# Performance work log

Measured on AMD Instinct MI355X. Metric: run time of the kernel, lower is better.

Reference implementation:

```python
import jax, jax.numpy as jnp
import numpy as np

B, S, E = 4, 2048, 768
DFF = 4 * E
EPS = 1e-5


def _layernorm(x, g, b):
    mu = jnp.mean(x, axis=-1, keepdims=True)
    var = jnp.mean(jnp.square(x - mu), axis=-1, keepdims=True)
    return (x - mu) * jax.lax.rsqrt(var + EPS) * g + b


def setup_inputs() -> dict:
    key = jax.random.key(0)
    ks = jax.random.split(key, 16)
    w = lambda k, shp: jax.random.normal(k, shp, dtype=jnp.float32) * 0.02
    inp = {
        "x": jax.random.normal(ks[0], (B, S, E), dtype=jnp.float32),
        "kv": jax.random.normal(ks[1], (B, S, E), dtype=jnp.float32),
        "wq_w": w(ks[2], (E, E)), "wq_b": jnp.zeros((E,), jnp.float32),
        "wk_w": w(ks[3], (E, E)), "wk_b": jnp.zeros((E,), jnp.float32),
        "wv_w": w(ks[4], (E, E)), "wv_b": jnp.zeros((E,), jnp.float32),
        "ln1_g": jnp.ones((E,), jnp.float32), "ln1_b": jnp.zeros((E,), jnp.float32),
        "wq2_w": w(ks[5], (E, E)), "wq2_b": jnp.zeros((E,), jnp.float32),
        "wk2_w": w(ks[6], (E, E)), "wk2_b": jnp.zeros((E,), jnp.float32),
        "wv2_w": w(ks[7], (E, E)), "wv2_b": jnp.zeros((E,), jnp.float32),
        "ln2_g": jnp.ones((E,), jnp.float32), "ln2_b": jnp.zeros((E,), jnp.float32),
        "w1": w(ks[8], (DFF, E)), "b1": jnp.zeros((DFF,), jnp.float32),
        "w2": w(ks[9], (E, DFF)), "b2": jnp.zeros((E,), jnp.float32),
        "ln3_g": jnp.ones((E,), jnp.float32), "ln3_b": jnp.zeros((E,), jnp.float32),
    }
    return inp


def reference(x, kv, wq_w, wq_b, wk_w, wk_b, wv_w, wv_b, ln1_g, ln1_b,
              wq2_w, wq2_b, wk2_w, wk2_b, wv2_w, wv2_b, ln2_g, ln2_b,
              w1, b1, w2, b2, ln3_g, ln3_b):
    scalar = 1.0 / np.sqrt(E).astype(np.float32)
    mask_value = jnp.finfo(x.dtype).min
    s = x.shape[1]
    causal = jnp.triu(jnp.ones((s, s), dtype=bool), k=1)  # True above diagonal -> masked

    # ---- causal self-attention (single head, full E) ----
    q = x @ wq_w.T + wq_b
    k = x @ wk_w.T + wk_b
    v = x @ wv_w.T + wv_b
    scores = jnp.einsum('bqe,bke->bqk', q, k) * scalar
    scores = jnp.where(causal, mask_value, scores)
    h1 = jnp.einsum('bqk,bke->bqe', jax.nn.softmax(scores, axis=-1), v)
    x = _layernorm(x + h1, ln1_g, ln1_b)

    # ---- cross-attention over kv (no mask) ----
    q2 = x @ wq2_w.T + wq2_b
    k2 = kv @ wk2_w.T + wk2_b
    v2 = kv @ wv2_w.T + wv2_b
    scores2 = jnp.einsum('bqe,bke->bqk', q2, k2) * scalar
    h2 = jnp.einsum('bqk,bke->bqe', jax.nn.softmax(scores2, axis=-1), v2)
    x = _layernorm(x + h2, ln2_g, ln2_b)

    # ---- MLP: Linear -> ReLU -> Linear -> ReLU (note trailing ReLU) ----
    h = jax.nn.relu(x @ w1.T + b1)
    mlp = jax.nn.relu(h @ w2.T + b2)
    return _layernorm(x + mlp, ln3_g, ln3_b)
```

## Files before the change

kernel.cpp:

```cpp
#include <hip/hip_runtime.h>
#include <hip/hip_bf16.h>
#include <math.h>


typedef __bf16 bf16_t;
typedef bf16_t bf16x4 __attribute__((ext_vector_type(4)));
typedef bf16_t bf16x8 __attribute__((ext_vector_type(8)));
typedef float f32x4 __attribute__((ext_vector_type(4)));

struct MMDesc {
    const bf16_t* A;
    const bf16_t* B;
    const float* bias;
    __hip_bfloat16* C;
    float* lsum;
    int koff;
    int trans;
};
struct MMArgs { MMDesc g[8]; };

__device__ __forceinline__ int xcd_swz(int bid, int nwg) {
    const int q = nwg >> 3, r = nwg & 7;
    const int xcd = bid & 7, o = bid >> 3;
    const int base = (xcd < r) ? xcd * (q + 1) : r * (q + 1) + (xcd - r) * q;
    return base + o;
}

__device__ __forceinline__ void load16(const bf16_t* g, bf16_t* l) {
    __builtin_amdgcn_global_load_lds(
        (const __attribute__((address_space(1))) unsigned int*)g,
        (__attribute__((address_space(3))) unsigned int*)l, 16, 0, 0);
}

#define SBAR asm volatile("s_barrier" ::: "memory")
#define SCH  __builtin_amdgcn_sched_barrier(0)
#define PRIO1 __builtin_amdgcn_s_setprio(1)
#define PRIO0 __builtin_amdgcn_s_setprio(0)
#define VMC0 asm volatile("s_waitcnt vmcnt(0)" ::: "memory")

#define RDA(dst, base, H) do { \
    _Pragma("unroll") \
    for (int i_ = 0; i_ < 4; ++i_) \
        dst[i_] = *(const bf16x8*)((base) + (H) + i_ * 1024); \
} while (0)
#define RDB(dst, base) do { \
    dst[0] = *(const bf16x8*)(base); \
    dst[1] = *(const bf16x8*)((base) + 1024); \
    dst[2] = *(const bf16x8*)((base) + 8192); \
    dst[3] = *(const bf16x8*)((base) + 8192 + 1024); \
} while (0)
#define CL16(mh, A_, B_) do { \
    _Pragma("unroll") \
    for (int mi = 0; mi < 4; ++mi) \
    _Pragma("unroll") \
    for (int nj = 0; nj < 4; ++nj) \
        acc[(mh) * 4 + mi][nj] = __builtin_amdgcn_mfma_f32_16x16x32_bf16( \
            A_[mi], B_[nj], acc[(mh) * 4 + mi][nj], 0, 0, 0); \
} while (0)
#define PH(nr) do { \
    __builtin_amdgcn_sched_group_barrier(0x100, nr, 0); \
    __builtin_amdgcn_sched_group_barrier(0x008, 16, 0); \
    SCH; \
} while (0)

__device__ __forceinline__ void mm8_core(
    const bf16_t* Ag, const bf16_t* Bg, int lda, int ldb, int K,
    bf16_t* lds, int w, int l, f32x4 acc[8][4])
{
    const long ldal = lda, ldbl = ldb;
    const int fr = l & 15, kq = l >> 4;
    const int rr = w * 8 + (l >> 3);
    const int c8e = ((l & 7) ^ (l >> 3)) * 8;
    const bf16_t* pA[2];
    const bf16_t* pB[2];
    pA[0] = Ag + (long)rr * ldal + c8e;
    pA[1] = pA[0] + 128 * ldal;
    pB[0] = Bg + (long)rr * ldbl + c8e;
    pB[1] = pB[0] + 128 * ldbl;
    const int s0 = ((0 + kq) ^ (fr & 7)) * 8;
    const int s1 = ((4 + kq) ^ (fr & 7)) * 8;
    const int arow = ((w >> 2) * 64 + fr) * 64;
    const int brow = ((w & 3) * 32 + fr) * 64;
    const bf16_t* A00 = lds + arow + s0;
    const bf16_t* A01 = lds + arow + s1;
    const bf16_t* A10 = lds + 32768 + arow + s0;
    const bf16_t* A11 = lds + 32768 + arow + s1;
    const bf16_t* B00 = lds + 16384 + brow + s0;
    const bf16_t* B01 = lds + 16384 + brow + s1;
    const bf16_t* B10 = lds + 49152 + brow + s0;
    const bf16_t* B11 = lds + 49152 + brow + s1;
    bf16_t* stA = lds + w * 512;
    bf16_t* stB = lds + 16384 + w * 512;

    auto stg = [&](int b, int isB, int h, int t) {
        const bf16_t* g = (isB ? pB[h] : pA[h]) + (long)t * 64;
        bf16_t* d = (isB ? stB : stA) + b * 32768 + h * 8192;
        load16(g, d);
        load16(g + 64 * (isB ? ldbl : ldal), d + 4096);
    };

    bf16x8 a0[4], a1[4], b0[4], b1[4];
    const int NT = K >> 6, NI = NT >> 1;

    stg(0, 0, 0, 0); stg(0, 1, 0, 0); stg(0, 0, 1, 0); stg(0, 1, 1, 0);
    stg(1, 0, 0, 1); stg(1, 1, 0, 1);
    asm volatile("s_waitcnt vmcnt(4)" ::: "memory");
    SBAR; SCH;
    RDA(a0, A00, 0); RDB(b0, B00);
    SCH;

    for (int i = 0; i < NI; ++i) {
        const int tn1 = 2 * i + 1;
        int tn2 = 2 * i + 2; if (tn2 >= NT) tn2 -= 2;
        int tn3 = 2 * i + 3; if (tn3 >= NT) tn3 -= 2;
        RDA(a1, A01, 0); RDB(b1, B01);
        stg(1, 0, 1, tn1); stg(1, 1, 1, tn1);
        PRIO1; CL16(0, a0, b0); PRIO0;
        PH(8);
        RDA(a0, A00, 8192);
        PRIO1; CL16(0, a1, b1); PRIO0;
        PH(4);
        RDA(a1, A01, 8192);
        PRIO1; CL16(1, a0, b0); PRIO0;
        PH(4);
        VMC0;
        SBAR; SCH;
        stg(0, 0, 0, tn2); stg(0, 1, 0, tn2);
        RDA(a0, A10, 0); RDB(b0, B10);
        PRIO1; CL16(1, a1, b1); PRIO0;
        PH(8);
        RDA(a1, A11, 0); RDB(b1, B11);
        stg(0, 0, 1, tn2); stg(0, 1, 1, tn2);
        PRIO1; CL16(0, a0, b0); PRIO0;
        PH(8);
        RDA(a0, A10, 8192);
        PRIO1; CL16(0, a1, b1); PRIO0;
        PH(4);
        RDA(a1, A11, 8192);
        PRIO1; CL16(1, a0, b0); PRIO0;
        PH(4);
        VMC0;
        SBAR; SCH;
        stg(1, 0, 0, tn3); stg(1, 1, 0, tn3);
        RDA(a0, A00, 0); RDB(b0, B00);
        PRIO1; CL16(1, a1, b1); PRIO0;
        PH(8);
    }
    VMC0;
    SBAR; SCH;
}

template <bool RELU, bool CLAMPK>
__global__ __launch_bounds__(512, 2) void mm8_std(
    MMArgs args, int M, int N, int K, int lda, int ldb, float scale, int GX)
{
    __shared__ __align__(16) bf16_t lds[65536];
    const MMDesc dsc = args.g[blockIdx.z];

    const int lin = xcd_swz(blockIdx.x, gridDim.x);
    const int panel = lin / (8 * GX);
    const int rem = lin - panel * 8 * GX;
    const int bx = rem >> 3;
    const int by = panel * 8 + (rem & 7);
    const int m0 = by * 256, n0 = bx * 256;
    const int tid = threadIdx.x, w = tid >> 6, l = tid & 63;

    f32x4 acc[8][4];
    const f32x4 z4 = {0.f, 0.f, 0.f, 0.f};
#pragma unroll
    for (int i = 0; i < 8; ++i)
#pragma unroll
        for (int j = 0; j < 4; ++j) acc[i][j] = z4;

    int Keff = K;
    if (CLAMPK) {
        int km = (by + 1) * 256 - dsc.koff;
        Keff = km < K ? km : K;
    }
    if (!CLAMPK || Keff > 0)
        mm8_core(dsc.A + (long)m0 * lda, dsc.B + (long)n0 * ldb,
                 lda, ldb, Keff, lds, w, l, acc);

    const int fr = l & 15, erow = (l >> 4) * 4;
    const int wrow = (w >> 2) * 64, wcol = (w & 3) * 32;
    bf16_t* ctb = lds;
    __hip_bfloat16* ct = (__hip_bfloat16*)lds;
#pragma unroll
    for (int mh = 0; mh < 2; ++mh) {
        if (mh) __syncthreads();
#pragma unroll
        for (int nh = 0; nh < 2; ++nh)
#pragma unroll
            for (int ni = 0; ni < 2; ++ni) {
                const int cl = nh * 128 + wcol + ni * 16 + fr;
                const float bv = dsc.bias ? dsc.bias[n0 + cl] : 0.f;
#pragma unroll
                for (int mi = 0; mi < 4; ++mi) {
                    const int lr = wrow + mi * 16 + erow;
                    const f32x4 a = acc[mh * 4 + mi][nh * 2 + ni];
                    if (dsc.trans) {
                        bf16x4 p;
#pragma unroll
                        for (int r = 0; r < 4; ++r) {
                            float v = a[r] * scale + bv;
                            if (RELU) v = fmaxf(v, 0.f);
                            p[r] = (bf16_t)v;
                        }
                        *(bf16x4*)(ctb + cl * 140 + lr) = p;
                    } else {
#pragma unroll
                        for (int r = 0; r < 4; ++r) {
                            float v = a[r] * scale + bv;
                            if (RELU) v = fmaxf(v, 0.f);
                            ct[(lr + r) * 264 + cl] = __float2bfloat16(v);
                        }
                    }
                }
            }
        __syncthreads();
        if (dsc.trans) {
            __hip_bfloat16* base = dsc.C + ((long)(m0 >> 11) * N + n0) * 2048
                                 + (m0 & 2047) + mh * 128;
#pragma unroll
            for (int u = 0; u < 8; ++u) {
                const int e = u * 4096 + tid * 8;
                const int rl = e >> 7, cl = e & 127;
                const bf16_t* src = ctb + rl * 140 + cl;
                const uint2 lo = *(const uint2*)(src);
                const uint2 hi = *(const uint2*)(src + 4);
                const uint4 v = {lo.x, lo.y, hi.x, hi.y};
                *(uint4*)(base + (long)rl * 2048 + cl) = v;
            }
        } else {
            __hip_bfloat16* base = dsc.C + (long)(m0 + mh * 128) * N + n0;
#pragma unroll
            for (int u = 0; u < 8; ++u) {
                const int e = u * 4096 + tid * 8;
                *(uint4*)(base + (long)(e >> 8) * N + (e & 255))
                    = *(const uint4*)(ct + (e >> 8) * 264 + (e & 255));
            }
        }
    }
}

template <bool CAUSAL>
__global__ __launch_bounds__(512, 2) void mm8_exp(
    MMArgs args, int N, int K, int lda, int ldb, float scale, int GX)
{
    __shared__ __align__(16) bf16_t lds[65536];
    const MMDesc dsc = args.g[blockIdx.z];

    int bx, by;
    if (CAUSAL) {
        const int t = xcd_swz(blockIdx.x, gridDim.x);
        by = (int)((sqrtf(8.f * t + 1.f) - 1.f) * 0.5f);
        while ((by + 1) * (by + 2) / 2 <= t) ++by;
        while (by * (by + 1) / 2 > t) --by;
        bx = t - by * (by + 1) / 2;
    } else {
        const int lin = xcd_swz(blockIdx.x, gridDim.x);
        const int panel = lin / (8 * GX);
        const int rem = lin - panel * 8 * GX;
        bx = rem >> 3;
        by = panel * 8 + (rem & 7);
    }
    const int m0 = by * 256, n0 = bx * 256;
    const int tid = threadIdx.x, w = tid >> 6, l = tid & 63;

    f32x4 acc[8][4];
    const f32x4 z4 = {0.f, 0.f, 0.f, 0.f};
#pragma unroll
    for (int i = 0; i < 8; ++i)
#pragma unroll
        for (int j = 0; j < 4; ++j) acc[i][j] = z4;

    mm8_core(dsc.A + (long)m0 * lda, dsc.B + (long)n0 * ldb,
             lda, ldb, K, lds, w, l, acc);

    const int fr = l & 15, erow = (l >> 4) * 4;
    const int wrow = (w >> 2) * 64, wcol = (w & 3) * 32;
    __hip_bfloat16* ct = (__hip_bfloat16*)lds;
#pragma unroll
    for (int mh = 0; mh < 2; ++mh) {
        if (mh) __syncthreads();
#pragma unroll
        for (int mi = 0; mi < 4; ++mi) {
            const int lr = wrow + mi * 16 + erow;
#pragma unroll
            for (int r = 0; r < 4; ++r) {
                const int grow = m0 + mh * 128 + lr + r;
                float rs = 0.f;
#pragma unroll
                for (int nh = 0; nh < 2; ++nh)
#pragma unroll
                    for (int ni = 0; ni < 2; ++ni) {
                        const int cl = nh * 128 + wcol + ni * 16 + fr;
                        float e;
                        if (CAUSAL && (n0 + cl) > grow)
                            e = 0.f;
                        else
                            e = __expf(acc[mh * 4 + mi][nh * 2 + ni][r] * scale);
                        ct[(lr + r) * 264 + cl] = __float2bfloat16(e);
                        rs += e;
                    }
#pragma unroll
                for (int o = 8; o > 0; o >>= 1) rs += __shfl_down(rs, o, 16);
                if ((l & 15) == 0) atomicAdd(&dsc.lsum[grow], rs);
            }
        }
        __syncthreads();
        __hip_bfloat16* base = dsc.C + (long)(m0 + mh * 128) * N + n0;
#pragma unroll
        for (int u = 0; u < 8; ++u) {
            const int e = u * 4096 + tid * 8;
            *(uint4*)(base + (long)(e >> 8) * N + (e & 255))
                = *(const uint4*)(ct + (e >> 8) * 264 + (e & 255));
        }
    }
}

__device__ __forceinline__ float waveReduceSum(float v) {
#pragma unroll
    for (int o = 32; o > 0; o >>= 1) v += __shfl_down(v, o, 64);
    return v;
}
__device__ __forceinline__ float blockReduceSum(float v, float* s) {
    int lane = threadIdx.x & 63, w = threadIdx.x >> 6;
    v = waveReduceSum(v);
    __syncthreads();
    if (lane == 0) s[w] = v;
    __syncthreads();
    return s[0] + s[1] + s[2] + s[3];
}

template <bool BR, bool XF32>
__global__ __launch_bounds__(256) void ln_kernel(
    const float* __restrict__ xf, const __hip_bfloat16* __restrict__ xh,
    const __hip_bfloat16* __restrict__ h1, const __hip_bfloat16* __restrict__ h2,
    const float* __restrict__ hbias, const float* __restrict__ lsum,
    const float* __restrict__ g, const float* __restrict__ beta,
    float* __restrict__ outf, __hip_bfloat16* __restrict__ outb) {
    __shared__ float red[4];
    const int E = 768;
    const long row = blockIdx.x;
    const float hscale = lsum ? (1.f / lsum[row]) : 1.f;

    float vals[3];
    float sum = 0.f;
#pragma unroll
    for (int i = 0; i < 3; ++i) {
        int c = threadIdx.x + i * 256;
        float t = __bfloat162float(h1[row * E + c]) + __bfloat162float(h2[row * E + c]);
        if (BR) t = fmaxf(t + hbias[c], 0.f);
        else t *= hscale;
        float xv = XF32 ? xf[row * E + c] : __bfloat162float(xh[row * E + c]);
        vals[i] = xv + t;
        sum += vals[i];
    }
    sum = blockReduceSum(sum, red);
    const float mean = sum * (1.f / 768.f);

    float ss = 0.f;
#pragma unroll
    for (int i = 0; i < 3; ++i) {
        float d = vals[i] - mean;
        ss += d * d;
    }
    ss = blockReduceSum(ss, red);
    const float inv = rsqrtf(ss * (1.f / 768.f) + 1e-5f);

#pragma unroll
    for (int i = 0; i < 3; ++i) {
        int c = threadIdx.x + i * 256;
        float v = (vals[i] - mean) * inv * g[c] + beta[c];
        if (outf) outf[row * E + c] = v;
        if (outb) outb[row * E + c] = __float2bfloat16(v);
    }
}

struct CvtPtrs {
    const float* s[10];
    __hip_bfloat16* d[10];
    float* zero;
};
__global__ __launch_bounds__(256) void cvt_all(CvtPtrs p) {
    int bid = blockIdx.x, seg, off;
    if (bid >= 20352) {
        int i = (bid - 20352) * 1024 + threadIdx.x * 4;
        float4 z = {0.f, 0.f, 0.f, 0.f};
        *(float4*)(p.zero + i) = z;
        return;
    }
    if (bid < 3456) {
        seg = bid / 576;
        off = (bid % 576) * 1024;
    } else if (bid < 8064) {
        int t = bid - 3456;
        seg = 6 + t / 2304;
        off = (t % 2304) * 1024;
    } else {
        int t = bid - 8064;
        seg = 8 + t / 6144;
        off = (t % 6144) * 1024;
    }
    const float* s = p.s[seg];
    __hip_bfloat16* d = p.d[seg];
    int i = off + threadIdx.x * 4;
    float4 v = *(const float4*)(s + i);
    d[i + 0] = __float2bfloat16(v.x);
    d[i + 1] = __float2bfloat16(v.y);
    d[i + 2] = __float2bfloat16(v.z);
    d[i + 3] = __float2bfloat16(v.w);
}

extern "C" void kernel_launch(void* const* d_in, const int* in_sizes, int n_in,
                              void* d_out, int out_size, void* d_ws, size_t ws_size,
                              hipStream_t stream) {
    const int Bb = 4, S = 2048, E = 768, DFF = 3072;
    const int Nr = Bb * S;

    const float* x    = (const float*)d_in[0];
    const float* kv   = (const float*)d_in[1];
    const float* wq_w = (const float*)d_in[2];
    const float* wq_b = (const float*)d_in[3];
    const float* wk_w = (const float*)d_in[4];
    const float* wk_b = (const float*)d_in[5];
    const float* wv_w = (const float*)d_in[6];
    const float* wv_b = (const float*)d_in[7];
    const float* ln1g = (const float*)d_in[8];
    const float* ln1b = (const float*)d_in[9];
    const float* wq2w = (const float*)d_in[10];
    const float* wq2b = (const float*)d_in[11];
    const float* wk2w = (const float*)d_in[12];
    const float* wk2b = (const float*)d_in[13];
    const float* wv2w = (const float*)d_in[14];
    const float* wv2b = (const float*)d_in[15];
    const float* ln2g = (const float*)d_in[16];
    const float* ln2b = (const float*)d_in[17];
    const float* w1   = (const float*)d_in[18];
    const float* b1   = (const float*)d_in[19];
    const float* w2   = (const float*)d_in[20];
    const float* b2   = (const float*)d_in[21];
    const float* ln3g = (const float*)d_in[22];
    const float* ln3b = (const float*)d_in[23];
    float* out = (float*)d_out;

    char* wsp = (char*)d_ws;
    auto alloc = [&](size_t bytes) {
        char* p = wsp;
        wsp += (bytes + 255) & ~(size_t)255;
        return p;
    };
    const size_t nSE = (size_t)Nr * E;
    const size_t nSS = (size_t)Bb * S * S;
    __hip_bfloat16* Pb   = (__hip_bfloat16*)alloc(nSS * 2);
    __hip_bfloat16* qb   = (__hip_bfloat16*)alloc(nSE * 2);
    __hip_bfloat16* kb   = (__hip_bfloat16*)alloc(nSE * 2);
    __hip_bfloat16* hffb = Pb;
    __hip_bfloat16* vtb  = (__hip_bfloat16*)alloc(nSE * 2);
    __hip_bfloat16* xb   = (__hip_bfloat16*)alloc(nSE * 2);
    __hip_bfloat16* kvb  = (__hip_bfloat16*)alloc(nSE * 2);
    __hip_bfloat16* actb = (__hip_bfloat16*)alloc(nSE * 2);
    __hip_bfloat16* hA   = (__hip_bfloat16*)alloc(nSE * 2);
    __hip_bfloat16* hB   = (__hip_bfloat16*)alloc(nSE * 2);
    __hip_bfloat16* wqb   = (__hip_bfloat16*)alloc((size_t)E * E * 2);
    __hip_bfloat16* wkb   = (__hip_bfloat16*)alloc((size_t)E * E * 2);
    __hip_bfloat16* wvb   = (__hip_bfloat16*)alloc((size_t)E * E * 2);
    __hip_bfloat16* wq2bm = (__hip_bfloat16*)alloc((size_t)E * E * 2);
    __hip_bfloat16* wk2bm = (__hip_bfloat16*)alloc((size_t)E * E * 2);
    __hip_bfloat16* wv2bm = (__hip_bfloat16*)alloc((size_t)E * E * 2);
    __hip_bfloat16* w1b   = (__hip_bfloat16*)alloc((size_t)DFF * E * 2);
    __hip_bfloat16* w2b   = (__hip_bfloat16*)alloc((size_t)E * DFF * 2);
    float* lsum1 = (float*)alloc((size_t)Nr * 4);
    float* lsum2 = (float*)alloc((size_t)Nr * 4);

    __hip_bfloat16* k2b  = (__hip_bfloat16*)d_out;
    __hip_bfloat16* vtb2 = k2b + nSE;

    const float scale = 1.0f / sqrtf((float)E);
    const dim3 blk(256);
    const dim3 blk5(512);

    CvtPtrs cp;
    cp.s[0] = wq_w; cp.d[0] = wqb;
    cp.s[1] = wk_w; cp.d[1] = wkb;
    cp.s[2] = wv_w; cp.d[2] = wvb;
    cp.s[3] = wq2w; cp.d[3] = wq2bm;
    cp.s[4] = wk2w; cp.d[4] = wk2bm;
    cp.s[5] = wv2w; cp.d[5] = wv2bm;
    cp.s[6] = w1;   cp.d[6] = w1b;
    cp.s[7] = w2;   cp.d[7] = w2b;
    cp.s[8] = x;    cp.d[8] = xb;
    cp.s[9] = kv;   cp.d[9] = kvb;
    cp.zero = lsum1;
    cvt_all<<<8064 + 12288 + 16, blk, 0, stream>>>(cp);

    {
        MMArgs a{};
        a.g[0] = {(const bf16_t*)xb,  (const bf16_t*)wqb,   wq_b, qb,   nullptr, 0, 0};
        a.g[1] = {(const bf16_t*)xb,  (const bf16_t*)wkb,   wk_b, kb,   nullptr, 0, 0};
        a.g[2] = {(const bf16_t*)xb,  (const bf16_t*)wvb,   wv_b, vtb,  nullptr, 0, 1};
        a.g[3] = {(const bf16_t*)kvb, (const bf16_t*)wk2bm, wk2b, k2b,  nullptr, 0, 0};
        a.g[4] = {(const bf16_t*)kvb, (const bf16_t*)wv2bm, wv2b, vtb2, nullptr, 0, 1};
        mm8_std<false, false><<<dim3(96, 1, 5), blk5, 0, stream>>>(
            a, Nr, E, E, E, E, 1.f, 3);
    }
    {
        MMArgs a{};
        for (int b = 0; b < 4; ++b)
            a.g[b] = {(const bf16_t*)qb + (long)b * S * E,
                      (const bf16_t*)kb + (long)b * S * E, nullptr,
                      Pb + (long)b * S * S, lsum1 + b * S, 0, 0};
        mm8_exp<true><<<dim3(36, 1, 4), blk5, 0, stream>>>(a, S, E, E, E, scale, 8);
    }
    {
        MMArgs a{};
        for (int b = 0; b < 4; ++b)
            for (int ks = 0; ks < 2; ++ks)
                a.g[b * 2 + ks] = {(const bf16_t*)Pb + (long)b * S * S + ks * 1024,
                                   (const bf16_t*)vtb + (long)b * E * S + ks * 1024,
                                   nullptr, (ks ? hB : hA) + (long)b * S * E,
                                   nullptr, ks * 1024, 0};
        mm8_std<false, true><<<dim3(24, 1, 8), blk5, 0, stream>>>(
            a, S, E, 1024, S, S, 1.f, 3);
    }
    ln_kernel<false, false><<<Nr, blk, 0, stream>>>(
        nullptr, xb, hA, hB, nullptr, lsum1, ln1g, ln1b, nullptr, actb);

    {
        MMArgs a{};
        a.g[0] = {(const bf16_t*)actb, (const bf16_t*)wq2bm, wq2b, qb, nullptr, 0, 0};
        mm8_std<false, false><<<dim3(96, 1, 1), blk5, 0, stream>>>(
            a, Nr, E, E, E, E, 1.f, 3);
    }
    {
        MMArgs a{};
        for (int b = 0; b < 4; ++b)
            a.g[b] = {(const bf16_t*)qb + (long)b * S * E,
                      (const bf16_t*)k2b + (long)b * S * E, nullptr,
                      Pb + (long)b * S * S, lsum2 + b * S, 0, 0};
        mm8_exp<false><<<dim3(64, 1, 4), blk5, 0, stream>>>(a, S, E, E, E, scale, 8);
    }
    {
        MMArgs a{};
        for (int b = 0; b < 4; ++b)
            for (int ks = 0; ks < 2; ++ks)
                a.g[b * 2 + ks] = {(const bf16_t*)Pb + (long)b * S * S + ks * 1024,
                                   (const bf16_t*)vtb2 + (long)b * E * S + ks * 1024,
                                   nullptr, (ks ? hB : hA) + (long)b * S * E,
                                   nullptr, 0, 0};
        mm8_std<false, false><<<dim3(24, 1, 8), blk5, 0, stream>>>(
            a, S, E, 1024, S, S, 1.f, 3);
    }
    ln_kernel<false, false><<<Nr, blk, 0, stream>>>(
        nullptr, actb, hA, hB, nullptr, lsum2, ln2g, ln2b, nullptr, actb);

    {
        MMArgs a{};
        a.g[0] = {(const bf16_t*)actb, (const bf16_t*)w1b, b1, hffb, nullptr, 0, 0};
        mm8_std<true, false><<<dim3(384, 1, 1), blk5, 0, stream>>>(
            a, Nr, DFF, E, E, E, 1.f, 12);
    }
    {
        MMArgs a{};
        a.g[0] = {(const bf16_t*)hffb, (const bf16_t*)w2b, nullptr, hA, nullptr, 0, 0};
        a.g[1] = {(const bf16_t*)hffb + 1536, (const bf16_t*)w2b + 1536, nullptr,
                  hB, nullptr, 0, 0};
        mm8_std<false, false><<<dim3(96, 1, 2), blk5, 0, stream>>>(
            a, Nr, E, 1536, DFF, DFF, 1.f, 3);
    }
    ln_kernel<true, false><<<Nr, blk, 0, stream>>>(
        nullptr, actb, hA, hB, b2, nullptr, ln3g, ln3b, out, nullptr);
}
```

Measured before the change: 495.9 us.

## Shrink GEMM block tiles from 256x256 to 128x128 for more occupancy

```diff
diff --git a/kernel.cpp b/kernel.cpp
--- a/kernel.cpp
+++ b/kernel.cpp
@@ -38,123 +38,108 @@
 #define PRIO0 __builtin_amdgcn_s_setprio(0)
 #define VMC0 asm volatile("s_waitcnt vmcnt(0)" ::: "memory")
 
-#define RDA(dst, base, H) do { \
+#define RDA(dst, base) do { \
     _Pragma("unroll") \
     for (int i_ = 0; i_ < 4; ++i_) \
-        dst[i_] = *(const bf16x8*)((base) + (H) + i_ * 1024); \
+        dst[i_] = *(const bf16x8*)((base) + i_ * 1024); \
 } while (0)
 #define RDB(dst, base) do { \
     dst[0] = *(const bf16x8*)(base); \
     dst[1] = *(const bf16x8*)((base) + 1024); \
-    dst[2] = *(const bf16x8*)((base) + 8192); \
-    dst[3] = *(const bf16x8*)((base) + 8192 + 1024); \
 } while (0)
-#define CL16(mh, A_, B_) do { \
+#define CL8(A_, B_) do { \
     _Pragma("unroll") \
     for (int mi = 0; mi < 4; ++mi) \
     _Pragma("unroll") \
-    for (int nj = 0; nj < 4; ++nj) \
-        acc[(mh) * 4 + mi][nj] = __builtin_amdgcn_mfma_f32_16x16x32_bf16( \
-            A_[mi], B_[nj], acc[(mh) * 4 + mi][nj], 0, 0, 0); \
+    for (int nj = 0; nj < 2; ++nj) \
+        acc[mi][nj] = __builtin_amdgcn_mfma_f32_16x16x32_bf16( \
+            A_[mi], B_[nj], acc[mi][nj], 0, 0, 0); \
 } while (0)
-#define PH(nr) do { \
-    __builtin_amdgcn_sched_group_barrier(0x100, nr, 0); \
-    __builtin_amdgcn_sched_group_barrier(0x008, 16, 0); \
+#define PH6 do { \
+    __builtin_amdgcn_sched_group_barrier(0x100, 6, 0); \
+    __builtin_amdgcn_sched_group_barrier(0x008, 8, 0); \
     SCH; \
 } while (0)
 
 __device__ __forceinline__ void mm8_core(
     const bf16_t* Ag, const bf16_t* Bg, int lda, int ldb, int K,
-    bf16_t* lds, int w, int l, f32x4 acc[8][4])
+    bf16_t* lds, int w, int l, f32x4 acc[4][2])
 {
     const long ldal = lda, ldbl = ldb;
     const int fr = l & 15, kq = l >> 4;
     const int rr = w * 8 + (l >> 3);
     const int c8e = ((l & 7) ^ (l >> 3)) * 8;
-    const bf16_t* pA[2];
-    const bf16_t* pB[2];
-    pA[0] = Ag + (long)rr * ldal + c8e;
-    pA[1] = pA[0] + 128 * ldal;
-    pB[0] = Bg + (long)rr * ldbl + c8e;
-    pB[1] = pB[0] + 128 * ldbl;
+    const bf16_t* pA0 = Ag + (long)rr * ldal + c8e;
+    const bf16_t* pA1 = pA0 + 64 * ldal;
+    const bf16_t* pB0 = Bg + (long)rr * ldbl + c8e;
+    const bf16_t* pB1 = pB0 + 64 * ldbl;
     const int s0 = ((0 + kq) ^ (fr & 7)) * 8;
     const int s1 = ((4 + kq) ^ (fr & 7)) * 8;
     const int arow = ((w >> 2) * 64 + fr) * 64;
     const int brow = ((w & 3) * 32 + fr) * 64;
     const bf16_t* A00 = lds + arow + s0;
     const bf16_t* A01 = lds + arow + s1;
-    const bf16_t* A10 = lds + 32768 + arow + s0;
-    const bf16_t* A11 = lds + 32768 + arow + s1;
-    const bf16_t* B00 = lds + 16384 + brow + s0;
-    const bf16_t* B01 = lds + 16384 + brow + s1;
-    const bf16_t* B10 = lds + 49152 + brow + s0;
-    const bf16_t* B11 = lds + 49152 + brow + s1;
+    const bf16_t* A10 = lds + 16384 + arow + s0;
+    const bf16_t* A11 = lds + 16384 + arow + s1;
+    const bf16_t* B00 = lds + 8192 + brow + s0;
+    const bf16_t* B01 = lds + 8192 + brow + s1;
+    const bf16_t* B10 = lds + 24576 + brow + s0;
+    const bf16_t* B11 = lds + 24576 + brow + s1;
     bf16_t* stA = lds + w * 512;
-    bf16_t* stB = lds + 16384 + w * 512;
-
-    auto stg = [&](int b, int isB, int h, int t) {
-        const bf16_t* g = (isB ? pB[h] : pA[h]) + (long)t * 64;
-        bf16_t* d = (isB ? stB : stA) + b * 32768 + h * 8192;
-        load16(g, d);
-        load16(g + 64 * (isB ? ldbl : ldal), d + 4096);
+    bf16_t* stB = lds + 8192 + w * 512;
+
+    auto stg = [&](int b, int t) {
+        const bf16_t* ga = pA0 + (long)t * 64;
+        const bf16_t* gb = pB0 + (long)t * 64;
+        bf16_t* da = stA + b * 16384;
+        bf16_t* db = stB + b * 16384;
+        load16(ga, da);
+        load16(pA1 + (long)t * 64, da + 4096);
+        load16(gb, db);
+        load16(pB1 + (long)t * 64, db + 4096);
     };
 
-    bf16x8 a0[4], a1[4], b0[4], b1[4];
+    bf16x8 a0[4], a1[4], b0[2], b1[2];
     const int NT = K >> 6, NI = NT >> 1;
 
-    stg(0, 0, 0, 0); stg(0, 1, 0, 0); stg(0, 0, 1, 0); stg(0, 1, 1, 0);
-    stg(1, 0, 0, 1); stg(1, 1, 0, 1);
+    stg(0, 0);
+    stg(1, 1);
     asm volatile("s_waitcnt vmcnt(4)" ::: "memory");
     SBAR; SCH;
-    RDA(a0, A00, 0); RDB(b0, B00);
+    RDA(a0, A00); RDB(b0, B00);
     SCH;
 
     for (int i = 0; i < NI; ++i) {
-        const int tn1 = 2 * i + 1;
-        int tn2 = 2 * i + 2; if (tn2 >= NT) tn2 -= 2;
-        int tn3 = 2 * i + 3; if (tn3 >= NT) tn3 -= 2;
-        RDA(a1, A01, 0); RDB(b1, B01);
-        stg(1, 0, 1, tn1); stg(1, 1, 1, tn1);
-        PRIO1; CL16(0, a0, b0); PRIO0;
-        PH(8);
-        RDA(a0, A00, 8192);
-        PRIO1; CL16(0, a1, b1); PRIO0;
-        PH(4);
-        RDA(a1, A01, 8192);
-        PRIO1; CL16(1, a0, b0); PRIO0;
-        PH(4);
+        int t2 = 2 * i + 2; if (t2 >= NT) t2 -= 2;
+        int t3 = 2 * i + 3; if (t3 >= NT) t3 -= 2;
+        RDA(a1, A01); RDB(b1, B01);
+        PRIO1; CL8(a0, b0); PRIO0;
+        PH6;
         VMC0;
         SBAR; SCH;
-        stg(0, 0, 0, tn2); stg(0, 1, 0, tn2);
-        RDA(a0, A10, 0); RDB(b0, B10);
-        PRIO1; CL16(1, a1, b1); PRIO0;
-        PH(8);
-        RDA(a1, A11, 0); RDB(b1, B11);
-        stg(0, 0, 1, tn2); stg(0, 1, 1, tn2);
-        PRIO1; CL16(0, a0, b0); PRIO0;
-        PH(8);
-        RDA(a0, A10, 8192);
-        PRIO1; CL16(0, a1, b1); PRIO0;
-        PH(4);
-        RDA(a1, A11, 8192);
-        PRIO1; CL16(1, a0, b0); PRIO0;
-        PH(4);
+        stg(0, t2);
+        RDA(a0, A10); RDB(b0, B10);
+        PRIO1; CL8(a1, b1); PRIO0;
+        PH6;
+        RDA(a1, A11); RDB(b1, B11);
+        PRIO1; CL8(a0, b0); PRIO0;
+        PH6;
         VMC0;
         SBAR; SCH;
-        stg(1, 0, 0, tn3); stg(1, 1, 0, tn3);
-        RDA(a0, A00, 0); RDB(b0, B00);
-        PRIO1; CL16(1, a1, b1); PRIO0;
-        PH(8);
+        stg(1, t3);
+        RDA(a0, A00); RDB(b0, B00);
+        PRIO1; CL8(a1, b1); PRIO0;
+        PH6;
     }
     VMC0;
     SBAR; SCH;
 }
 
 template <bool RELU, bool CLAMPK>
-__global__ __launch_bounds__(512, 2) void mm8_std(
+__global__ __launch_bounds__(512, 4) void mm8_std(
     MMArgs args, int M, int N, int K, int lda, int ldb, float scale, int GX)
 {
-    __shared__ __align__(16) bf16_t lds[65536];
+    __shared__ __align__(16) bf16_t lds[32768];
     const MMDesc dsc = args.g[blockIdx.z];
 
     const int lin = xcd_swz(blockIdx.x, gridDim.x);
@@ -162,19 +147,19 @@
     const int rem = lin - panel * 8 * GX;
     const int bx = rem >> 3;
     const int by = panel * 8 + (rem & 7);
-    const int m0 = by * 256, n0 = bx * 256;
+    const int m0 = by * 128, n0 = bx * 128;
     const int tid = threadIdx.x, w = tid >> 6, l = tid & 63;
 
-    f32x4 acc[8][4];
+    f32x4 acc[4][2];
     const f32x4 z4 = {0.f, 0.f, 0.f, 0.f};
 #pragma unroll
-    for (int i = 0; i < 8; ++i)
-#pragma unroll
-        for (int j = 0; j < 4; ++j) acc[i][j] = z4;
+    for (int i = 0; i < 4; ++i)
+#pragma unroll
+        for (int j = 0; j < 2; ++j) acc[i][j] = z4;
 
     int Keff = K;
     if (CLAMPK) {
-        int km = (by + 1) * 256 - dsc.koff;
+        int km = (by + 1) * 128 - dsc.koff;
         Keff = km < K ? km : K;
     }
     if (!CLAMPK || Keff > 0)
@@ -182,72 +167,64 @@
                  lda, ldb, Keff, lds, w, l, acc);
 
     const int fr = l & 15, erow = (l >> 4) * 4;
-    const int wrow = (w >> 2) * 64, wcol = (w & 3) * 32;
+    const int wm = (w >> 2) * 64, wn = (w & 3) * 32;
     bf16_t* ctb = lds;
     __hip_bfloat16* ct = (__hip_bfloat16*)lds;
 #pragma unroll
-    for (int mh = 0; mh < 2; ++mh) {
-        if (mh) __syncthreads();
-#pragma unroll
-        for (int nh = 0; nh < 2; ++nh)
-#pragma unroll
-            for (int ni = 0; ni < 2; ++ni) {
-                const int cl = nh * 128 + wcol + ni * 16 + fr;
-                const float bv = dsc.bias ? dsc.bias[n0 + cl] : 0.f;
-#pragma unroll
-                for (int mi = 0; mi < 4; ++mi) {
-                    const int lr = wrow + mi * 16 + erow;
-                    const f32x4 a = acc[mh * 4 + mi][nh * 2 + ni];
-                    if (dsc.trans) {
-                        bf16x4 p;
-#pragma unroll
-                        for (int r = 0; r < 4; ++r) {
-                            float v = a[r] * scale + bv;
-                            if (RELU) v = fmaxf(v, 0.f);
-                            p[r] = (bf16_t)v;
-                        }
-                        *(bf16x4*)(ctb + cl * 140 + lr) = p;
-                    } else {
-#pragma unroll
-                        for (int r = 0; r < 4; ++r) {
-                            float v = a[r] * scale + bv;
-                            if (RELU) v = fmaxf(v, 0.f);
-                            ct[(lr + r) * 264 + cl] = __float2bfloat16(v);
-                        }
-                    }
+    for (int nj = 0; nj < 2; ++nj) {
+        const int cl = wn + nj * 16 + fr;
+        const float bv = dsc.bias ? dsc.bias[n0 + cl] : 0.f;
+#pragma unroll
+        for (int mi = 0; mi < 4; ++mi) {
+            const int lr = wm + mi * 16 + erow;
+            const f32x4 a = acc[mi][nj];
+            if (dsc.trans) {
+                bf16x4 p;
+#pragma unroll
+                for (int r = 0; r < 4; ++r) {
+                    float v = a[r] * scale + bv;
+                    if (RELU) v = fmaxf(v, 0.f);
+                    p[r] = (bf16_t)v;
+                }
+                *(bf16x4*)(ctb + cl * 136 + lr) = p;
+            } else {
+#pragma unroll
+                for (int r = 0; r < 4; ++r) {
+                    float v = a[r] * scale + bv;
+                    if (RELU) v = fmaxf(v, 0.f);
+                    ct[(lr + r) * 136 + cl] = __float2bfloat16(v);
                 }
             }
-        __syncthreads();
-        if (dsc.trans) {
-            __hip_bfloat16* base = dsc.C + ((long)(m0 >> 11) * N + n0) * 2048
-                                 + (m0 & 2047) + mh * 128;
-#pragma unroll
-            for (int u = 0; u < 8; ++u) {
-                const int e = u * 4096 + tid * 8;
-                const int rl = e >> 7, cl = e & 127;
-                const bf16_t* src = ctb + rl * 140 + cl;
-                const uint2 lo = *(const uint2*)(src);
-                const uint2 hi = *(const uint2*)(src + 4);
-                const uint4 v = {lo.x, lo.y, hi.x, hi.y};
-                *(uint4*)(base + (long)rl * 2048 + cl) = v;
-            }
-        } else {
-            __hip_bfloat16* base = dsc.C + (long)(m0 + mh * 128) * N + n0;
-#pragma unroll
-            for (int u = 0; u < 8; ++u) {
-                const int e = u * 4096 + tid * 8;
-                *(uint4*)(base + (long)(e >> 8) * N + (e & 255))
-                    = *(const uint4*)(ct + (e >> 8) * 264 + (e & 255));
-            }
         }
     }
+    __syncthreads();
+    if (dsc.trans) {
+        __hip_bfloat16* base = dsc.C + ((long)(m0 >> 11) * N + n0) * 2048
+                             + (m0 & 2047);
+#pragma unroll
+        for (int u = 0; u < 4; ++u) {
+            const int e = u * 4096 + tid * 8;
+            const int ec = e >> 7, s = e & 127;
+            *(uint4*)(base + (long)ec * 2048 + s)
+                = *(const uint4*)(ct + ec * 136 + s);
+        }
+    } else {
+        __hip_bfloat16* base = dsc.C + (long)m0 * N + n0;
+#pragma unroll
+        for (int u = 0; u < 4; ++u) {
+            const int e = u * 4096 + tid * 8;
+            const int rl = e >> 7, cl = e & 127;
+            *(uint4*)(base + (long)rl * N + cl)
+                = *(const uint4*)(ct + rl * 136 + cl);
+        }
+    }
 }
 
 template <bool CAUSAL>
-__global__ __launch_bounds__(512, 2) void mm8_exp(
+__global__ __launch_bounds__(512, 4) void mm8_exp(
     MMArgs args, int N, int K, int lda, int ldb, float scale, int GX)
 {
-    __shared__ __align__(16) bf16_t lds[65536];
+    __shared__ __align__(16) bf16_t lds[32768];
     const MMDesc dsc = args.g[blockIdx.z];
 
     int bx, by;
@@ -264,58 +241,53 @@
         bx = rem >> 3;
         by = panel * 8 + (rem & 7);
     }
-    const int m0 = by * 256, n0 = bx * 256;
+    const int m0 = by * 128, n0 = bx * 128;
     const int tid = threadIdx.x, w = tid >> 6, l = tid & 63;
 
-    f32x4 acc[8][4];
+    f32x4 acc[4][2];
     const f32x4 z4 = {0.f, 0.f, 0.f, 0.f};
 #pragma unroll
-    for (int i = 0; i < 8; ++i)
-#pragma unroll
-        for (int j = 0; j < 4; ++j) acc[i][j] = z4;
+    for (int i = 0; i < 4; ++i)
+#pragma unroll
+        for (int j = 0; j < 2; ++j) acc[i][j] = z4;
 
     mm8_core(dsc.A + (long)m0 * lda, dsc.B + (long)n0 * ldb,
              lda, ldb, K, lds, w, l, acc);
 
     const int fr = l & 15, erow = (l >> 4) * 4;
-    const int wrow = (w >> 2) * 64, wcol = (w & 3) * 32;
+    const int wm = (w >> 2) * 64, wn = (w & 3) * 32;
     __hip_bfloat16* ct = (__hip_bfloat16*)lds;
 #pragma unroll
-    for (int mh = 0; mh < 2; ++mh) {
-        if (mh) __syncthreads();
-#pragma unroll
-        for (int mi = 0; mi < 4; ++mi) {
-            const int lr = wrow + mi * 16 + erow;
-#pragma unroll
-            for (int r = 0; r < 4; ++r) {
-                const int grow = m0 + mh * 128 + lr + r;
-                float rs = 0.f;
-#pragma unroll
-                for (int nh = 0; nh < 2; ++nh)
-#pragma unroll
-                    for (int ni = 0; ni < 2; ++ni) {
-                        const int cl = nh * 128 + wcol + ni * 16 + fr;
-                        float e;
-                        if (CAUSAL && (n0 + cl) > grow)
-                            e = 0.f;
-                        else
-                            e = __expf(acc[mh * 4 + mi][nh * 2 + ni][r] * scale);
-                        ct[(lr + r) * 264 + cl] = __float2bfloat16(e);
-                        rs += e;
-                    }
-#pragma unroll
-                for (int o = 8; o > 0; o >>= 1) rs += __shfl_down(rs, o, 16);
-                if ((l & 15) == 0) atomicAdd(&dsc.lsum[grow], rs);
+    for (int mi = 0; mi < 4; ++mi) {
+        const int lr = wm + mi * 16 + erow;
+#pragma unroll
+        for (int r = 0; r < 4; ++r) {
+            const int grow = m0 + lr + r;
+            float rs = 0.f;
+#pragma unroll
+            for (int nj = 0; nj < 2; ++nj) {
+                const int cl = wn + nj * 16 + fr;
+                float e;
+                if (CAUSAL && (n0 + cl) > grow)
+                    e = 0.f;
+                else
+                    e = __expf(acc[mi][nj][r] * scale);
+                ct[(lr + r) * 136 + cl] = __float2bfloat16(e);
+                rs += e;
             }
+#pragma unroll
+            for (int o = 8; o > 0; o >>= 1) rs += __shfl_down(rs, o, 16);
+            if ((l & 15) == 0) atomicAdd(&dsc.lsum[grow], rs);
         }
-        __syncthreads();
-        __hip_bfloat16* base = dsc.C + (long)(m0 + mh * 128) * N + n0;
-#pragma unroll
-        for (int u = 0; u < 8; ++u) {
-            const int e = u * 4096 + tid * 8;
-            *(uint4*)(base + (long)(e >> 8) * N + (e & 255))
-                = *(const uint4*)(ct + (e >> 8) * 264 + (e & 255));
-        }
+    }
+    __syncthreads();
+    __hip_bfloat16* base = dsc.C + (long)m0 * N + n0;
+#pragma unroll
+    for (int u = 0; u < 4; ++u) {
+        const int e = u * 4096 + tid * 8;
+        const int rl = e >> 7, cl = e & 127;
+        *(uint4*)(base + (long)rl * N + cl)
+            = *(const uint4*)(ct + rl * 136 + cl);
     }
 }
 
@@ -502,8 +474,8 @@
         a.g[2] = {(const bf16_t*)xb,  (const bf16_t*)wvb,   wv_b, vtb,  nullptr, 0, 1};
         a.g[3] = {(const bf16_t*)kvb, (const bf16_t*)wk2bm, wk2b, k2b,  nullptr, 0, 0};
         a.g[4] = {(const bf16_t*)kvb, (const bf16_t*)wv2bm, wv2b, vtb2, nullptr, 0, 1};
-        mm8_std<false, false><<<dim3(96, 1, 5), blk5, 0, stream>>>(
-            a, Nr, E, E, E, E, 1.f, 3);
+        mm8_std<false, false><<<dim3(384, 1, 5), blk5, 0, stream>>>(
+            a, Nr, E, E, E, E, 1.f, 6);
     }
     {
         MMArgs a{};
@@ -511,7 +483,7 @@
             a.g[b] = {(const bf16_t*)qb + (long)b * S * E,
                       (const bf16_t*)kb + (long)b * S * E, nullptr,
                       Pb + (long)b * S * S, lsum1 + b * S, 0, 0};
-        mm8_exp<true><<<dim3(36, 1, 4), blk5, 0, stream>>>(a, S, E, E, E, scale, 8);
+        mm8_exp<true><<<dim3(136, 1, 4), blk5, 0, stream>>>(a, S, E, E, E, scale, 16);
     }
     {
         MMArgs a{};
@@ -521,8 +493,8 @@
                                    (const bf16_t*)vtb + (long)b * E * S + ks * 1024,
                                    nullptr, (ks ? hB : hA) + (long)b * S * E,
                                    nullptr, ks * 1024, 0};
-        mm8_std<false, true><<<dim3(24, 1, 8), blk5, 0, stream>>>(
-            a, S, E, 1024, S, S, 1.f, 3);
+        mm8_std<false, true><<<dim3(96, 1, 8), blk5, 0, stream>>>(
+            a, S, E, 1024, S, S, 1.f, 6);
     }
     ln_kernel<false, false><<<Nr, blk, 0, stream>>>(
         nullptr, xb, hA, hB, nullptr, lsum1, ln1g, ln1b, nullptr, actb);
@@ -530,8 +502,8 @@
     {
         MMArgs a{};
         a.g[0] = {(const bf16_t*)actb, (const bf16_t*)wq2bm, wq2b, qb, nullptr, 0, 0};
-        mm8_std<false, false><<<dim3(96, 1, 1), blk5, 0, stream>>>(
-            a, Nr, E, E, E, E, 1.f, 3);
+        mm8_std<false, false><<<dim3(384, 1, 1), blk5, 0, stream>>>(
+            a, Nr, E, E, E, E, 1.f, 6);
     }
     {
         MMArgs a{};
@@ -539,7 +511,7 @@
             a.g[b] = {(const bf16_t*)qb + (long)b * S * E,
                       (const bf16_t*)k2b + (long)b * S * E, nullptr,
                       Pb + (long)b * S * S, lsum2 + b * S, 0, 0};
-        mm8_exp<false><<<dim3(64, 1, 4), blk5, 0, stream>>>(a, S, E, E, E, scale, 8);
+        mm8_exp<false><<<dim3(256, 1, 4), blk5, 0, stream>>>(a, S, E, E, E, scale, 16);
     }
     {
         MMArgs a{};
@@ -549,8 +521,8 @@
                                    (const bf16_t*)vtb2 + (long)b * E * S + ks * 1024,
                                    nullptr, (ks ? hB : hA) + (long)b * S * E,
                                    nullptr, 0, 0};
-        mm8_std<false, false><<<dim3(24, 1, 8), blk5, 0, stream>>>(
-            a, S, E, 1024, S, S, 1.f, 3);
+        mm8_std<false, false><<<dim3(96, 1, 8), blk5, 0, stream>>>(
+            a, S, E, 1024, S, S, 1.f, 6);
     }
     ln_kernel<false, false><<<Nr, blk, 0, stream>>>(
         nullptr, actb, hA, hB, nullptr, lsum2, ln2g, ln2b, nullptr, actb);
@@ -558,16 +530,16 @@
     {
         MMArgs a{};
         a.g[0] = {(const bf16_t*)actb, (const bf16_t*)w1b, b1, hffb, nullptr, 0, 0};
-        mm8_std<true, false><<<dim3(384, 1, 1), blk5, 0, stream>>>(
-            a, Nr, DFF, E, E, E, 1.f, 12);
+        mm8_std<true, false><<<dim3(1536, 1, 1), blk5, 0, stream>>>(
+            a, Nr, DFF, E, E, E, 1.f, 24);
     }
     {
         MMArgs a{};
         a.g[0] = {(const bf16_t*)hffb, (const bf16_t*)w2b, nullptr, hA, nullptr, 0, 0};
         a.g[1] = {(const bf16_t*)hffb + 1536, (const bf16_t*)w2b + 1536, nullptr,
                   hB, nullptr, 0, 0};
-        mm8_std<false, false><<<dim3(96, 1, 2), blk5, 0, stream>>>(
-            a, Nr, E, 1536, DFF, DFF, 1.f, 3);
+        mm8_std<false, false><<<dim3(384, 1, 2), blk5, 0, stream>>>(
+            a, Nr, E, 1536, DFF, DFF, 1.f, 6);
     }
     ln_kernel<true, false><<<Nr, blk, 0, stream>>>(
         nullptr, actb, hA, hB, b2, nullptr, ln3g, ln3b, out, nullptr);
```

Result: slower. 520.9 us (+5.1%).

## Add 128x128-tile GEMM kernel and use it for smaller projections and FFN1

Applied to the files above, without the earlier changes.

```diff
diff --git a/kernel.cpp b/kernel.cpp
--- a/kernel.cpp
+++ b/kernel.cpp
@@ -38,12 +38,12 @@
 #define PRIO0 __builtin_amdgcn_s_setprio(0)
 #define VMC0 asm volatile("s_waitcnt vmcnt(0)" ::: "memory")
 
-#define RDA(dst, base, H) do { \
+#define RDA4(dst, base, H) do { \
     _Pragma("unroll") \
     for (int i_ = 0; i_ < 4; ++i_) \
         dst[i_] = *(const bf16x8*)((base) + (H) + i_ * 1024); \
 } while (0)
-#define RDB(dst, base) do { \
+#define RDB4(dst, base) do { \
     dst[0] = *(const bf16x8*)(base); \
     dst[1] = *(const bf16x8*)((base) + 1024); \
     dst[2] = *(const bf16x8*)((base) + 8192); \
@@ -106,45 +106,142 @@
     stg(1, 0, 0, 1); stg(1, 1, 0, 1);
     asm volatile("s_waitcnt vmcnt(4)" ::: "memory");
     SBAR; SCH;
-    RDA(a0, A00, 0); RDB(b0, B00);
+    RDA4(a0, A00, 0); RDB4(b0, B00);
     SCH;
 
     for (int i = 0; i < NI; ++i) {
         const int tn1 = 2 * i + 1;
         int tn2 = 2 * i + 2; if (tn2 >= NT) tn2 -= 2;
         int tn3 = 2 * i + 3; if (tn3 >= NT) tn3 -= 2;
-        RDA(a1, A01, 0); RDB(b1, B01);
+        RDA4(a1, A01, 0); RDB4(b1, B01);
         stg(1, 0, 1, tn1); stg(1, 1, 1, tn1);
         PRIO1; CL16(0, a0, b0); PRIO0;
         PH(8);
-        RDA(a0, A00, 8192);
+        RDA4(a0, A00, 8192);
         PRIO1; CL16(0, a1, b1); PRIO0;
         PH(4);
-        RDA(a1, A01, 8192);
+        RDA4(a1, A01, 8192);
         PRIO1; CL16(1, a0, b0); PRIO0;
         PH(4);
         VMC0;
         SBAR; SCH;
         stg(0, 0, 0, tn2); stg(0, 1, 0, tn2);
-        RDA(a0, A10, 0); RDB(b0, B10);
+        RDA4(a0, A10, 0); RDB4(b0, B10);
         PRIO1; CL16(1, a1, b1); PRIO0;
         PH(8);
-        RDA(a1, A11, 0); RDB(b1, B11);
+        RDA4(a1, A11, 0); RDB4(b1, B11);
         stg(0, 0, 1, tn2); stg(0, 1, 1, tn2);
         PRIO1; CL16(0, a0, b0); PRIO0;
         PH(8);
-        RDA(a0, A10, 8192);
+        RDA4(a0, A10, 8192);
         PRIO1; CL16(0, a1, b1); PRIO0;
         PH(4);
-        RDA(a1, A11, 8192);
+        RDA4(a1, A11, 8192);
         PRIO1; CL16(1, a0, b0); PRIO0;
         PH(4);
         VMC0;
         SBAR; SCH;
         stg(1, 0, 0, tn3); stg(1, 1, 0, tn3);
-        RDA(a0, A00, 0); RDB(b0, B00);
+        RDA4(a0, A00, 0); RDB4(b0, B00);
         PRIO1; CL16(1, a1, b1); PRIO0;
         PH(8);
+    }
+    VMC0;
+    SBAR; SCH;
+}
+
+#define RDA2(dst, base) do { \
+    _Pragma("unroll") \
+    for (int i_ = 0; i_ < 4; ++i_) \
+        dst[i_] = *(const bf16x8*)((base) + i_ * 1024); \
+} while (0)
+#define RDB2(dst, base) do { \
+    dst[0] = *(const bf16x8*)(base); \
+    dst[1] = *(const bf16x8*)((base) + 1024); \
+} while (0)
+#define CL8(A_, B_) do { \
+    _Pragma("unroll") \
+    for (int mi = 0; mi < 4; ++mi) \
+    _Pragma("unroll") \
+    for (int nj = 0; nj < 2; ++nj) \
+        acc[mi][nj] = __builtin_amdgcn_mfma_f32_16x16x32_bf16( \
+            A_[mi], B_[nj], acc[mi][nj], 0, 0, 0); \
+} while (0)
+#define PH6 do { \
+    __builtin_amdgcn_sched_group_barrier(0x100, 6, 0); \
+    __builtin_amdgcn_sched_group_barrier(0x008, 8, 0); \
+    SCH; \
+} while (0)
+
+__device__ __forceinline__ void mm4_core(
+    const bf16_t* Ag, const bf16_t* Bg, int lda, int ldb, int K,
+    bf16_t* lds, int w, int l, f32x4 acc[4][2])
+{
+    const long ldal = lda, ldbl = ldb;
+    const int fr = l & 15, kq = l >> 4;
+    const int rr = w * 8 + (l >> 3);
+    const int c8e = ((l & 7) ^ (l >> 3)) * 8;
+    const bf16_t* pA0 = Ag + (long)rr * ldal + c8e;
+    const bf16_t* pA1 = pA0 + 64 * ldal;
+    const bf16_t* pB0 = Bg + (long)rr * ldbl + c8e;
+    const bf16_t* pB1 = pB0 + 64 * ldbl;
+    const int s0 = ((0 + kq) ^ (fr & 7)) * 8;
+    const int s1 = ((4 + kq) ^ (fr & 7)) * 8;
+    const int arow = ((w >> 2) * 64 + fr) * 64;
+    const int brow = ((w & 3) * 32 + fr) * 64;
+    const bf16_t* A00 = lds + arow + s0;
+    const bf16_t* A01 = lds + arow + s1;
+    const bf16_t* A10 = lds + 16384 + arow + s0;
+    const bf16_t* A11 = lds + 16384 + arow + s1;
+    const bf16_t* B00 = lds + 8192 + brow + s0;
+    const bf16_t* B01 = lds + 8192 + brow + s1;
+    const bf16_t* B10 = lds + 24576 + brow + s0;
+    const bf16_t* B11 = lds + 24576 + brow + s1;
+    bf16_t* stA = lds + w * 512;
+    bf16_t* stB = lds + 8192 + w * 512;
+
+    auto stg = [&](int b, int t) {
+        const bf16_t* ga = pA0 + (long)t * 64;
+        const bf16_t* gb = pB0 + (long)t * 64;
+        bf16_t* da = stA + b * 16384;
+        bf16_t* db = stB + b * 16384;
+        load16(ga, da);
+        load16(pA1 + (long)t * 64, da + 4096);
+        load16(gb, db);
+        load16(pB1 + (long)t * 64, db + 4096);
+    };
+
+    bf16x8 a0[4], a1[4], b0[2], b1[2];
+    const int NT = K >> 6, NI = NT >> 1;
+
+    stg(0, 0);
+    stg(1, 1);
+    asm volatile("s_waitcnt vmcnt(4)" ::: "memory");
+    SBAR; SCH;
+    RDA2(a0, A00); RDB2(b0, B00);
+    SCH;
+
+    for (int i = 0; i < NI; ++i) {
+        int t2 = 2 * i + 2; if (t2 >= NT) t2 -= 2;
+        int t3 = 2 * i + 3; if (t3 >= NT) t3 -= 2;
+        RDA2(a1, A01); RDB2(b1, B01);
+        PRIO1; CL8(a0, b0); PRIO0;
+        PH6;
+        VMC0;
+        SBAR; SCH;
+        stg(0, t2);
+        RDA2(a0, A10); RDB2(b0, B10);
+        PRIO1; CL8(a1, b1); PRIO0;
+        PH6;
+        RDA2(a1, A11); RDB2(b1, B11);
+        PRIO1; CL8(a0, b0); PRIO0;
+        PH6;
+        VMC0;
+        SBAR; SCH;
+        stg(1, t3);
+        RDA2(a0, A00); RDB2(b0, B00);
+        PRIO1; CL8(a1, b1); PRIO0;
+        PH6;
     }
     VMC0;
     SBAR; SCH;
@@ -316,6 +413,67 @@
             *(uint4*)(base + (long)(e >> 8) * N + (e & 255))
                 = *(const uint4*)(ct + (e >> 8) * 264 + (e & 255));
         }
+    }
+}
+
+template <bool RELU, bool CLAMPK>
+__global__ __launch_bounds__(512, 4) void mm4_std(
+    MMArgs args, int M, int N, int K, int lda, int ldb, float scale, int GX)
+{
+    __shared__ __align__(16) bf16_t lds[32768];
+    const MMDesc dsc = args.g[blockIdx.z];
+
+    const int lin = xcd_swz(blockIdx.x, gridDim.x);
+    const int panel = lin / (8 * GX);
+    const int rem = lin - panel * 8 * GX;
+    const int bx = rem >> 3;
+    const int by = panel * 8 + (rem & 7);
+    const int m0 = by * 128, n0 = bx * 128;
+    const int tid = threadIdx.x, w = tid >> 6, l = tid & 63;
+
+    f32x4 acc[4][2];
+    const f32x4 z4 = {0.f, 0.f, 0.f, 0.f};
+#pragma unroll
+    for (int i = 0; i < 4; ++i)
+#pragma unroll
+        for (int j = 0; j < 2; ++j) acc[i][j] = z4;
+
+    int Keff = K;
+    if (CLAMPK) {
+        int km = (by + 1) * 128 - dsc.koff;
+        Keff = km < K ? km : K;
+    }
+    if (!CLAMPK || Keff > 0)
+        mm4_core(dsc.A + (long)m0 * lda, dsc.B + (long)n0 * ldb,
+                 lda, ldb, Keff, lds, w, l, acc);
+
+    const int fr = l & 15, erow = (l >> 4) * 4;
+    const int wm = (w >> 2) * 64, wn = (w & 3) * 32;
+    __hip_bfloat16* ct = (__hip_bfloat16*)lds;
+#pragma unroll
+    for (int nj = 0; nj < 2; ++nj) {
+        const int cl = wn + nj * 16 + fr;
+        const float bv = dsc.bias ? dsc.bias[n0 + cl] : 0.f;
+#pragma unroll
+        for (int mi = 0; mi < 4; ++mi) {
+            const int lr = wm + mi * 16 + erow;
+            const f32x4 a = acc[mi][nj];
+#pragma unroll
+            for (int r = 0; r < 4; ++r) {
+                float v = a[r] * scale + bv;
+                if (RELU) v = fmaxf(v, 0.f);
+                ct[(lr + r) * 136 + cl] = __float2bfloat16(v);
+            }
+        }
+    }
+    __syncthreads();
+    __hip_bfloat16* base = dsc.C + (long)m0 * N + n0;
+#pragma unroll
+    for (int u = 0; u < 4; ++u) {
+        const int e = u * 4096 + tid * 8;
+        const int rl = e >> 7, cl = e & 127;
+        *(uint4*)(base + (long)rl * N + cl)
+            = *(const uint4*)(ct + rl * 136 + cl);
     }
 }
 
@@ -521,8 +679,8 @@
                                    (const bf16_t*)vtb + (long)b * E * S + ks * 1024,
                                    nullptr, (ks ? hB : hA) + (long)b * S * E,
                                    nullptr, ks * 1024, 0};
-        mm8_std<false, true><<<dim3(24, 1, 8), blk5, 0, stream>>>(
-            a, S, E, 1024, S, S, 1.f, 3);
+        mm4_std<false, true><<<dim3(96, 1, 8), blk5, 0, stream>>>(
+            a, S, E, 1024, S, S, 1.f, 6);
     }
     ln_kernel<false, false><<<Nr, blk, 0, stream>>>(
         nullptr, xb, hA, hB, nullptr, lsum1, ln1g, ln1b, nullptr, actb);
@@ -530,8 +688,8 @@
     {
         MMArgs a{};
         a.g[0] = {(const bf16_t*)actb, (const bf16_t*)wq2bm, wq2b, qb, nullptr, 0, 0};
-        mm8_std<false, false><<<dim3(96, 1, 1), blk5, 0, stream>>>(
-            a, Nr, E, E, E, E, 1.f, 3);
+        mm4_std<false, false><<<dim3(384, 1, 1), blk5, 0, stream>>>(
+            a, Nr, E, E, E, E, 1.f, 6);
     }
     {
         MMArgs a{};
@@ -558,8 +716,8 @@
     {
         MMArgs a{};
         a.g[0] = {(const bf16_t*)actb, (const bf16_t*)w1b, b1, hffb, nullptr, 0, 0};
-        mm8_std<true, false><<<dim3(384, 1, 1), blk5, 0, stream>>>(
-            a, Nr, DFF, E, E, E, 1.f, 12);
+        mm4_std<true, false><<<dim3(1536, 1, 1), blk5, 0, stream>>>(
+            a, Nr, DFF, E, E, E, 1.f, 24);
     }
     {
         MMArgs a{};
```

After: 457.6 us. -7.7%, faster.
